# Optimization experiments

Hardware: AMD Instinct MI355X
Metric: run time of the kernel (lower is better)

The kernel has to match this reference:

```python
import jax, jax.numpy as jnp
import numpy as np

NUM_TREES = 256
DEPTH = 6
BATCH = 4096
FEATURES = 256


def setup_inputs() -> dict:
    key = jax.random.key(0)
    k1, k2, k3 = jax.random.split(key, 3)
    inputs = jax.random.normal(k1, (BATCH, FEATURES), dtype=jnp.float32)
    # Keras 'random_normal' initializer: stddev 0.05
    decision_weights = 0.05 * jax.random.normal(k2, (NUM_TREES, DEPTH, FEATURES), dtype=jnp.float32)
    thresholds = jnp.zeros((NUM_TREES, DEPTH), dtype=jnp.float32)
    leaf_weights = 0.05 * jax.random.normal(k3, (NUM_TREES, 2 ** DEPTH), dtype=jnp.float32)
    return {
        'inputs': inputs,
        'decision_weights': decision_weights,
        'thresholds': thresholds,
        'leaf_weights': leaf_weights,
    }


def reference(inputs, decision_weights, thresholds, leaf_weights):
    # Faithful to tf.einsum('bj,tdk->btd'): j and k are NOT shared, so both
    # are independently summed -> outer product of per-row sum and per-(t,d) sum.
    decisions = jnp.einsum('bj,tdk->btd', inputs, decision_weights)  # [B,T,D]
    decisions = jax.nn.sigmoid(decisions + thresholds)
    B = inputs.shape[0]
    T = decision_weights.shape[0]
    depth = decision_weights.shape[1]
    paths = jnp.ones((B, T, 1), dtype=inputs.dtype)
    for d in range(depth):  # loop over small fixed depth (structural)
        dl = decisions[:, :, d:d + 1]  # [B,T,1]
        paths = jnp.concatenate([paths * dl, paths * (1.0 - dl)], axis=2)
    outputs = jnp.einsum('btl,tl->bt', paths, leaf_weights)  # [B,T]
    return jnp.mean(outputs, axis=1, keepdims=True)  # [B,1]
```

## Files before the change

### kernel.cpp

```cpp
#include <hip/hip_runtime.h>
#include <hip/hip_bf16.h>


#define NUM_TREES 256
#define DEPTH 6
#define LEAVES 64
#define BATCH 4096
#define FEATURES 256
#define BPB 4

__global__ __launch_bounds__(256) void rowsum_kernel(
    const float* __restrict__ inputs,
    const float* __restrict__ dw,
    float* __restrict__ s_in,
    float* __restrict__ s_w)
{
    const int wave = (blockIdx.x * blockDim.x + threadIdx.x) >> 6;
    const int lane = threadIdx.x & 63;
    const float* src;
    float* dst;
    if (wave < BATCH) {
        src = inputs + (size_t)wave * FEATURES;
        dst = s_in + wave;
    } else {
        const int r = wave - BATCH;
        src = dw + (size_t)r * FEATURES;
        dst = s_w + r;
    }
    float4 v = reinterpret_cast<const float4*>(src)[lane];
    float s = (v.x + v.y) + (v.z + v.w);
#pragma unroll
    for (int off = 32; off > 0; off >>= 1)
        s += __shfl_down(s, off);
    if (lane == 0) *dst = s;
}

__global__ __launch_bounds__(256) void forest_kernel(
    const float* __restrict__ thr,
    const float* __restrict__ leaf,
    const float* __restrict__ s_in,
    const float* __restrict__ s_w,
    float* __restrict__ out)
{
    const int t  = threadIdx.x;
    const int b0 = blockIdx.x * BPB;

    float sw[DEPTH], th[DEPTH];
#pragma unroll
    for (int d = 0; d < DEPTH; ++d) {
        sw[d] = s_w[t * DEPTH + d];
        th[d] = thr[t * DEPTH + d];
    }
    float lf[LEAVES];
    const float4* lp = reinterpret_cast<const float4*>(leaf + (size_t)t * LEAVES);
#pragma unroll
    for (int i = 0; i < LEAVES / 4; ++i) {
        float4 v = lp[i];
        lf[4 * i + 0] = v.x; lf[4 * i + 1] = v.y;
        lf[4 * i + 2] = v.z; lf[4 * i + 3] = v.w;
    }

    float res[BPB];
#pragma unroll
    for (int bi = 0; bi < BPB; ++bi) {
        const float si = s_in[b0 + bi];
        float dec[DEPTH];
#pragma unroll
        for (int d = 0; d < DEPTH; ++d) {
            const float x = fmaf(si, sw[d], th[d]);
            dec[d] = 1.0f / (1.0f + __expf(-x));
        }
        float m[32];
#pragma unroll
        for (int i = 0; i < 32; ++i) m[i] = fmaf(dec[5], lf[i] - lf[i + 32], lf[i + 32]);
#pragma unroll
        for (int i = 0; i < 16; ++i) m[i] = fmaf(dec[4], m[i] - m[i + 16], m[i + 16]);
#pragma unroll
        for (int i = 0; i < 8; ++i)  m[i] = fmaf(dec[3], m[i] - m[i + 8],  m[i + 8]);
#pragma unroll
        for (int i = 0; i < 4; ++i)  m[i] = fmaf(dec[2], m[i] - m[i + 4],  m[i + 4]);
#pragma unroll
        for (int i = 0; i < 2; ++i)  m[i] = fmaf(dec[1], m[i] - m[i + 2],  m[i + 2]);
        res[bi] = fmaf(dec[0], m[0] - m[1], m[1]);
    }

    __shared__ float red[4][BPB];
    const int lane = t & 63;
    const int wv   = t >> 6;
#pragma unroll
    for (int bi = 0; bi < BPB; ++bi) {
        float v = res[bi];
#pragma unroll
        for (int off = 32; off > 0; off >>= 1)
            v += __shfl_down(v, off);
        if (lane == 0) red[wv][bi] = v;
    }
    __syncthreads();
    if (t < BPB) {
        const float v = red[0][t] + red[1][t] + red[2][t] + red[3][t];
        out[b0 + t] = v * (1.0f / (float)NUM_TREES);
    }
}

extern "C" void kernel_launch(void* const* d_in, const int* in_sizes, int n_in,
                              void* d_out, int out_size, void* d_ws, size_t ws_size,
                              hipStream_t stream) {
    const float* inputs = (const float*)d_in[0];
    const float* dw     = (const float*)d_in[1];
    const float* thr    = (const float*)d_in[2];
    const float* leaf   = (const float*)d_in[3];
    float* out = (float*)d_out;

    float* s_in = (float*)d_ws;
    float* s_w  = s_in + BATCH;

    const int total_waves = BATCH + NUM_TREES * DEPTH;
    rowsum_kernel<<<total_waves / 4, 256, 0, stream>>>(inputs, dw, s_in, s_w);

    forest_kernel<<<BATCH / BPB, 256, 0, stream>>>(thr, leaf, s_in, s_w, out);
}
```

Before: 72.69 us.

## Transpose per-tree params into coalesced workspace layout and double batch rows per block

Result: faster. 69.63 us (-4.2%).

```diff
diff --git a/kernel.cpp b/kernel.cpp
--- a/kernel.cpp
+++ b/kernel.cpp
@@ -7,39 +7,59 @@
 #define LEAVES 64
 #define BATCH 4096
 #define FEATURES 256
-#define BPB 4
+#define BPB 8
 
-__global__ __launch_bounds__(256) void rowsum_kernel(
+#define WS_SIN  0
+#define WS_SWT  4096
+#define WS_THT  5632
+#define WS_LF4  7168
+
+__global__ __launch_bounds__(256) void prep_kernel(
     const float* __restrict__ inputs,
     const float* __restrict__ dw,
-    float* __restrict__ s_in,
-    float* __restrict__ s_w)
+    const float* __restrict__ thr,
+    const float* __restrict__ leaf,
+    float* __restrict__ ws)
 {
-    const int wave = (blockIdx.x * blockDim.x + threadIdx.x) >> 6;
+    const int gw   = (blockIdx.x * blockDim.x + threadIdx.x) >> 6;
     const int lane = threadIdx.x & 63;
-    const float* src;
-    float* dst;
-    if (wave < BATCH) {
-        src = inputs + (size_t)wave * FEATURES;
-        dst = s_in + wave;
+
+    if (gw < BATCH + NUM_TREES * DEPTH) {
+        const float* src;
+        float* dst;
+        if (gw < BATCH) {
+            src = inputs + (size_t)gw * FEATURES;
+            dst = ws + WS_SIN + gw;
+        } else {
+            const int r = gw - BATCH;
+            const int t = r / DEPTH;
+            const int d = r - t * DEPTH;
+            src = dw + (size_t)r * FEATURES;
+            dst = ws + WS_SWT + d * NUM_TREES + t;
+        }
+        float4 v = reinterpret_cast<const float4*>(src)[lane];
+        float s = (v.x + v.y) + (v.z + v.w);
+#pragma unroll
+        for (int off = 32; off > 0; off >>= 1)
+            s += __shfl_down(s, off);
+        if (lane == 0) *dst = s;
+    } else if (gw < BATCH + NUM_TREES * DEPTH + 64) {
+        const int j = gw - (BATCH + NUM_TREES * DEPTH);
+        const int c = j >> 2;
+        const int t = ((j & 3) << 6) | lane;
+        float4 v = reinterpret_cast<const float4*>(leaf)[t * (LEAVES / 4) + c];
+        reinterpret_cast<float4*>(ws + WS_LF4)[c * NUM_TREES + t] = v;
     } else {
-        const int r = wave - BATCH;
-        src = dw + (size_t)r * FEATURES;
-        dst = s_w + r;
+        const int j = gw - (BATCH + NUM_TREES * DEPTH + 64);
+        const int idx = j * 64 + lane;
+        const int t = idx / DEPTH;
+        const int d = idx - t * DEPTH;
+        ws[WS_THT + d * NUM_TREES + t] = thr[idx];
     }
-    float4 v = reinterpret_cast<const float4*>(src)[lane];
-    float s = (v.x + v.y) + (v.z + v.w);
-#pragma unroll
-    for (int off = 32; off > 0; off >>= 1)
-        s += __shfl_down(s, off);
-    if (lane == 0) *dst = s;
 }
 
 __global__ __launch_bounds__(256) void forest_kernel(
-    const float* __restrict__ thr,
-    const float* __restrict__ leaf,
-    const float* __restrict__ s_in,
-    const float* __restrict__ s_w,
+    const float* __restrict__ ws,
     float* __restrict__ out)
 {
     const int t  = threadIdx.x;
@@ -48,22 +68,22 @@
     float sw[DEPTH], th[DEPTH];
 #pragma unroll
     for (int d = 0; d < DEPTH; ++d) {
-        sw[d] = s_w[t * DEPTH + d];
-        th[d] = thr[t * DEPTH + d];
+        sw[d] = ws[WS_SWT + d * NUM_TREES + t];
+        th[d] = ws[WS_THT + d * NUM_TREES + t];
     }
     float lf[LEAVES];
-    const float4* lp = reinterpret_cast<const float4*>(leaf + (size_t)t * LEAVES);
+    const float4* lp = reinterpret_cast<const float4*>(ws + WS_LF4);
 #pragma unroll
-    for (int i = 0; i < LEAVES / 4; ++i) {
-        float4 v = lp[i];
-        lf[4 * i + 0] = v.x; lf[4 * i + 1] = v.y;
-        lf[4 * i + 2] = v.z; lf[4 * i + 3] = v.w;
+    for (int c = 0; c < LEAVES / 4; ++c) {
+        float4 v = lp[c * NUM_TREES + t];
+        lf[4 * c + 0] = v.x; lf[4 * c + 1] = v.y;
+        lf[4 * c + 2] = v.z; lf[4 * c + 3] = v.w;
     }
 
     float res[BPB];
 #pragma unroll
     for (int bi = 0; bi < BPB; ++bi) {
-        const float si = s_in[b0 + bi];
+        const float si = ws[WS_SIN + b0 + bi];
         float dec[DEPTH];
 #pragma unroll
         for (int d = 0; d < DEPTH; ++d) {
@@ -110,12 +130,9 @@
     const float* thr    = (const float*)d_in[2];
     const float* leaf   = (const float*)d_in[3];
     float* out = (float*)d_out;
+    float* ws  = (float*)d_ws;
 
-    float* s_in = (float*)d_ws;
-    float* s_w  = s_in + BATCH;
+    prep_kernel<<<1430, 256, 0, stream>>>(inputs, dw, thr, leaf, ws);
 
-    const int total_waves = BATCH + NUM_TREES * DEPTH;
-    rowsum_kernel<<<total_waves / 4, 256, 0, stream>>>(inputs, dw, s_in, s_w);
-
-    forest_kernel<<<BATCH / BPB, 256, 0, stream>>>(thr, leaf, s_in, s_w, out);
+    forest_kernel<<<BATCH / BPB, 256, 0, stream>>>(ws, out);
 }
```
